# Optimization experiments

Measured on AMD Instinct MI355X. Metric: run time of the kernel, lower is better.

Reference implementation:

```python
import jax, jax.numpy as jnp
import numpy as np

N = 49104   # anchors (from hardcoded [2, 49104, 80] in source)
C = 80      # classes
K = 100     # max detections kept per class (fixed for jit-able output shapes)
SCORE_THRESH = 0.05
IOU_THRESH = 0.5


def setup_inputs() -> dict:
    key = jax.random.key(0)
    k1, k2 = jax.random.split(key)
    scores = jax.random.uniform(k1, (N, C), dtype=jnp.float32)
    # build valid xyxy boxes inside an ~800x800 image
    r = jax.random.uniform(k2, (N, 4), dtype=jnp.float32)
    x1 = r[:, 0] * 768.0
    y1 = r[:, 1] * 768.0
    w = r[:, 2] * 96.0 + 4.0
    h = r[:, 3] * 96.0 + 4.0
    boxes = jnp.stack([x1, y1, x1 + w, y1 + h], axis=1)
    return {"scores": scores, "boxes": boxes}


def _nms_all(scores, boxes):
    """Per-class greedy NMS, vectorized over classes via vmap.
    scores: [N, C], boxes: [N, 4] xyxy. Returns idxs/scs/valid each [C, K]."""
    areas = (boxes[:, 2] - boxes[:, 0]) * (boxes[:, 3] - boxes[:, 1])  # [N]

    def iou_vs_all(b, b_area):  # b: [4]
        ix1 = jnp.maximum(b[0], boxes[:, 0])
        iy1 = jnp.maximum(b[1], boxes[:, 1])
        ix2 = jnp.minimum(b[2], boxes[:, 2])
        iy2 = jnp.minimum(b[3], boxes[:, 3])
        inter = jnp.clip(ix2 - ix1, 0.0) * jnp.clip(iy2 - iy1, 0.0)
        return inter / (b_area + areas - inter + 1e-8)  # [N]

    def nms_one_class(s_c):  # s_c: [N]
        # score threshold (matches `scores > 0.05` masking in the torch loop)
        s0 = jnp.where(s_c > SCORE_THRESH, s_c, -jnp.inf)

        def step(s, _):
            idx = jnp.argmax(s)
            sc = s[idx]
            keep = jnp.isfinite(sc)  # anything left above threshold?
            ious = iou_vs_all(boxes[idx], areas[idx])
            suppress = (ious > IOU_THRESH) & keep
            s_next = jnp.where(suppress, -jnp.inf, s).at[idx].set(-jnp.inf)
            return s_next, (idx, sc, keep)

        _, (idxs, scs, keeps) = jax.lax.scan(step, s0, None, length=K)
        return idxs, scs, keeps  # each [K]

    return jax.vmap(nms_one_class)(scores.T)  # map over C classes


def reference(scores, boxes):
    idxs, scs, valids = _nms_all(scores, boxes)  # [C, K] each
    idxs = idxs.reshape(-1)                       # [C*K]
    valids = valids.reshape(-1)                   # [C*K] bool
    final_scores = jnp.where(valids, scs.reshape(-1), 0.0)        # [C*K]
    final_classes = jnp.repeat(jnp.arange(C, dtype=jnp.int32), K)  # [C*K]
    final_boxes = boxes[idxs] * valids[:, None].astype(boxes.dtype)  # [C*K, 4]
    return final_scores, final_classes, final_boxes, valids
```

## Files before the change

### kernel.cpp

```cpp
#include <hip/hip_runtime.h>
#include <math.h>
#include <stdint.h>

#define N_ANCH 49104
#define NCLS 80
#define KDET 100
#define CAP 256
#define TPB 256
#define NBINS 1024
#define NBLK 240
#define SUBCAP 32
#define THETA 0.996090f
#define QTOT (N_ANCH * NCLS / 4)
#define QPB (QTOT / NBLK)
#define JMAX 16

#define LIST_ELEMS ((size_t)NCLS * NBLK * SUBCAP)
#define SUBCNT_OFF (LIST_ELEMS * 8)
#define WS_NEED (SUBCNT_OFF + (size_t)NCLS * NBLK * 4)

__global__ __launch_bounds__(TPB) void collect_kernel(const float* __restrict__ scores,
                                                      uint64_t* __restrict__ list,
                                                      int* __restrict__ subcnt) {
    const int blk = blockIdx.x, tid = threadIdx.x;
    __shared__ int lcnt[NCLS];
    for (int c = tid; c < NCLS; c += TPB) lcnt[c] = 0;
    __syncthreads();
    const float4* sc4 = (const float4*)scores;
    const int q0 = blk * QPB;
    for (int q = q0 + tid; q < q0 + QPB; q += TPB) {
        float4 v = sc4[q];
        int n = q / 20;
        int c0 = 4 * (q % 20);
        float ss[4] = {v.x, v.y, v.z, v.w};
#pragma unroll
        for (int u = 0; u < 4; u++) {
            float s = ss[u];
            if (s > THETA) {
                int c = c0 + u;
                int p = atomicAdd(&lcnt[c], 1);
                if (p < SUBCAP) {
                    uint32_t bits = __float_as_uint(s);
                    list[((size_t)c * NBLK + blk) * SUBCAP + p] =
                        ((uint64_t)(~bits) << 16) | (uint64_t)n;
                }
            }
        }
    }
    __syncthreads();
    for (int c = tid; c < NCLS; c += TPB) subcnt[c * NBLK + blk] = lcnt[c];
}

struct ChunkShared {
    uint64_t keys[CAP];
    float4   rbox[CAP];
    float    ra[CAP], rs[CAP];
    uint64_t smat[CAP * (CAP / 64)];
    uint64_t lwbuf[CAP / 64];
    uint64_t s_kw[CAP / 64];
    int      s_cw[4];
    float4   kbox[KDET];
    float    kar[KDET], ksc[KDET];
};

__device__ __forceinline__ int process_chunk(ChunkShared& S, int tid, int M, int kc0,
                                             const float* __restrict__ boxes) {
    if (M <= 0) return kc0;
    const int lane = tid & 63, wid = tid >> 6;
    uint64_t key = (tid < M) ? S.keys[tid] : ~0ull;
    for (int k = 2; k <= CAP; k <<= 1) {
        for (int j = k >> 1; j > 0; j >>= 1) {
            uint64_t other;
            if (j >= 64) {
                __syncthreads();
                S.keys[tid] = key;
                __syncthreads();
                other = S.keys[tid ^ j];
            } else {
                other = (uint64_t)__shfl_xor((unsigned long long)key, j, 64);
            }
            const bool up = ((tid & k) == 0);
            const bool lower = ((tid & j) == 0);
            const uint64_t mn = key < other ? key : other;
            const uint64_t mx = key < other ? other : key;
            key = (lower == up) ? mn : mx;
        }
    }
    if (tid < M) {
        int n = (int)(key & 0xFFFFull);
        float4 bx = *(const float4*)(boxes + (size_t)n * 4);
        S.rbox[tid] = bx;
        S.ra[tid] = (bx.z - bx.x) * (bx.w - bx.y);
        S.rs[tid] = __uint_as_float(~((uint32_t)(key >> 16)));
    }
    __syncthreads();
    bool alive = (tid < M);
    if (alive && kc0 > 0) {
        float4 b = S.rbox[tid];
        float arb = S.ra[tid];
        for (int k2 = 0; k2 < kc0; k2++) {
            float4 kb = S.kbox[k2];
            float ix1 = fmaxf(kb.x, b.x), iy1 = fmaxf(kb.y, b.y);
            float ix2 = fminf(kb.z, b.z), iy2 = fminf(kb.w, b.w);
            float inter = fmaxf(ix2 - ix1, 0.0f) * fmaxf(iy2 - iy1, 0.0f);
            float iou = inter / (S.kar[k2] + arb - inter + 1e-8f);
            if (iou > 0.5f) { alive = false; break; }
        }
    }
    {
        uint64_t bal = __ballot(alive);
        if (lane == 0) S.lwbuf[wid] = bal;
    }
    __syncthreads();
    for (int p = wid; p < 10; p += 4) {
        const int vw = (int)((0x3333222110ull >> (4 * p)) & 0xF);
        const int ws = (int)((0x3210210100ull >> (4 * p)) & 0xF);
        const int i0 = vw << 6;
        if (i0 >= M) continue;
        const int i1 = min(M, i0 + 64);
        const int jj = (ws << 6) + lane;
        float4 bj = S.rbox[jj];
        float arj = S.ra[jj];
        for (int i = i0; i < i1; i++) {
            bool bit = false;
            if (jj < i) {
                float4 bi = S.rbox[i];
                float ari = S.ra[i];
                float ix1 = fmaxf(bj.x, bi.x), iy1 = fmaxf(bj.y, bi.y);
                float ix2 = fminf(bj.z, bi.z), iy2 = fminf(bj.w, bi.w);
                float inter = fmaxf(ix2 - ix1, 0.0f) * fmaxf(iy2 - iy1, 0.0f);
                float iou = inter / (arj + ari - inter + 1e-8f);
                bit = iou > 0.5f;
            }
            uint64_t bb = __ballot(bit);
            if (lane == 0) S.smat[((size_t)i << 2) + ws] = bb;
        }
    }
    __syncthreads();
    uint64_t st0 = 0, st1 = 0, st2 = 0, st3 = 0;
    if (tid < M) {
        st0 = S.smat[((size_t)tid << 2) + 0];
        if (wid >= 1) st1 = S.smat[((size_t)tid << 2) + 1];
        if (wid >= 2) st2 = S.smat[((size_t)tid << 2) + 2];
        if (wid >= 3) st3 = S.smat[((size_t)tid << 2) + 3];
    }
    bool kept = alive;
    bool converged = false;
    for (int it = 0; it < JMAX; it++) {
        uint64_t kb = __ballot(kept);
        if (lane == 0) S.s_kw[wid] = kb;
        __syncthreads();
        const uint64_t k0 = S.s_kw[0], k1 = S.s_kw[1], k2 = S.s_kw[2], k3 = S.s_kw[3];
        const bool sup = ((k0 & st0) | (k1 & st1) | (k2 & st2) | (k3 & st3)) != 0ull;
        const bool nk = alive && !sup;
        uint64_t cb = __ballot(nk != kept);
        if (lane == 0) S.s_cw[wid] = (cb != 0ull) ? 1 : 0;
        kept = nk;
        __syncthreads();
        if ((S.s_cw[0] | S.s_cw[1] | S.s_cw[2] | S.s_cw[3]) == 0) { converged = true; break; }
    }
    if (!converged) {
        if (tid == 0) {
            uint64_t lv[4] = {S.lwbuf[0], S.lwbuf[1], S.lwbuf[2], S.lwbuf[3]};
            uint64_t kw[4] = {0, 0, 0, 0};
            for (int i = 0; i < M; i++) {
                const int w = i >> 6, b = i & 63;
                if (!((lv[w] >> b) & 1ull)) continue;
                const uint64_t* row = &S.smat[(size_t)i << 2];
                uint64_t sup = kw[0] & row[0];
                if (w >= 1) sup |= kw[1] & row[1];
                if (w >= 2) sup |= kw[2] & row[2];
                if (w >= 3) sup |= kw[3] & row[3];
                if (!sup) kw[w] |= 1ull << b;
            }
            S.s_kw[0] = kw[0]; S.s_kw[1] = kw[1]; S.s_kw[2] = kw[2]; S.s_kw[3] = kw[3];
        }
        __syncthreads();
    }
    const uint64_t k0 = S.s_kw[0], k1 = S.s_kw[1], k2 = S.s_kw[2], k3 = S.s_kw[3];
    const int total = __popcll(k0) + __popcll(k1) + __popcll(k2) + __popcll(k3);
    const uint64_t mykw = (wid == 0) ? k0 : (wid == 1) ? k1 : (wid == 2) ? k2 : k3;
    if (tid < M && ((mykw >> lane) & 1ull)) {
        int rank = __popcll(mykw & ((1ull << lane) - 1ull));
        if (wid > 0) rank += __popcll(k0);
        if (wid > 1) rank += __popcll(k1);
        if (wid > 2) rank += __popcll(k2);
        const int r = kc0 + rank;
        if (r < KDET) { S.kbox[r] = S.rbox[tid]; S.kar[r] = S.ra[tid]; S.ksc[r] = S.rs[tid]; }
    }
    __syncthreads();
    return min(kc0 + total, KDET);
}

__global__ __launch_bounds__(TPB) void nms_final(const float* __restrict__ scores,
                                                 const float* __restrict__ boxes,
                                                 const uint64_t* __restrict__ list,
                                                 const int* __restrict__ subcnt,
                                                 int use_lists,
                                                 float* __restrict__ out) {
    const int c = blockIdx.x, tid = threadIdx.x;
    const int lane = tid & 63, wid = tid >> 6;
    __shared__ ChunkShared S;
    __shared__ int hist[NBINS];
    __shared__ int s_wtot[4];
    __shared__ int s_ov, s_cnt, s_lo;

    int kc = 0;
    bool fast = false;
    if (use_lists) {
        if (tid == 0) s_ov = 0;
        __syncthreads();
        int raw = (tid < NBLK) ? subcnt[c * NBLK + tid] : 0;
        if (raw > SUBCAP) atomicOr(&s_ov, 1);
        int v = min(raw, SUBCAP);
        int incl = v;
        for (int d = 1; d < 64; d <<= 1) {
            int o = __shfl_up(incl, d, 64);
            if (lane >= d) incl += o;
        }
        if (lane == 63) s_wtot[wid] = incl;
        __syncthreads();
        int woff = 0;
        for (int w = 0; w < wid; w++) woff += s_wtot[w];
        const int off = woff + incl - v;
        const int M0 = s_wtot[0] + s_wtot[1] + s_wtot[2] + s_wtot[3];
        fast = (s_ov == 0) && (M0 <= CAP);
        if (fast && tid < NBLK && v > 0) {
            const uint64_t* src = list + ((size_t)c * NBLK + tid) * SUBCAP;
            for (int k = 0; k < v; k++) S.keys[off + k] = src[k];
        }
        __syncthreads();
        if (fast) kc = process_chunk(S, tid, M0, 0, boxes);
    }
    if (kc < KDET) {
        const float hicut = fast ? THETA : 3.0e38f;
        if (!fast) kc = 0;
        for (int b = tid; b < NBINS; b += TPB) hist[b] = 0;
        __syncthreads();
        for (int n = tid; n < N_ANCH; n += TPB) {
            float s = scores[(size_t)n * NCLS + c];
            if (s > 0.05f && s <= hicut) {
                int b = (int)(s * 1024.0f);
                b = b < 0 ? 0 : (b > NBINS - 1 ? NBINS - 1 : b);
                atomicAdd(&hist[b], 1);
            }
        }
        __syncthreads();
        int hi = NBINS;
        while (hi > 0 && kc < KDET) {
            if (tid == 0) {
                int lo = hi, tot = 0;
                while (lo > 0 && tot + hist[lo - 1] <= CAP) { lo--; tot += hist[lo]; }
                if (lo == hi) lo = hi - 1;
                s_lo = lo; s_cnt = 0;
            }
            __syncthreads();
            const int lo = s_lo;
            for (int n = tid; n < N_ANCH; n += TPB) {
                float s = scores[(size_t)n * NCLS + c];
                if (s > 0.05f && s <= hicut) {
                    int b = (int)(s * 1024.0f);
                    b = b < 0 ? 0 : (b > NBINS - 1 ? NBINS - 1 : b);
                    if (b >= lo && b < hi) {
                        int p = atomicAdd(&s_cnt, 1);
                        if (p < CAP) {
                            uint32_t bits = __float_as_uint(s);
                            S.keys[p] = ((uint64_t)(~bits) << 16) | (uint64_t)n;
                        }
                    }
                }
            }
            __syncthreads();
            const int M2 = min(s_cnt, CAP);
            kc = process_chunk(S, tid, M2, kc, boxes);
            hi = lo;
        }
    }
    __syncthreads();

    float* o_sc = out;
    float* o_cl = out + NCLS * KDET;
    float* o_bx = out + 2 * NCLS * KDET;
    float* o_va = out + 6 * NCLS * KDET;
    for (int k = tid; k < KDET; k += TPB) {
        bool valid = k < kc;
        o_sc[c * KDET + k] = valid ? S.ksc[k] : 0.0f;
        o_cl[c * KDET + k] = (float)c;
        o_va[c * KDET + k] = valid ? 1.0f : 0.0f;
        float4 bo;
        if (valid) bo = S.kbox[k];
        else { bo.x = 0.0f; bo.y = 0.0f; bo.z = 0.0f; bo.w = 0.0f; }
        *(float4*)(o_bx + ((size_t)(c * KDET + k)) * 4) = bo;
    }
}

extern "C" void kernel_launch(void* const* d_in, const int* in_sizes, int n_in,
                              void* d_out, int out_size, void* d_ws, size_t ws_size,
                              hipStream_t stream) {
    const float* scores = (const float*)d_in[0];
    const float* boxes  = (const float*)d_in[1];
    float* out = (float*)d_out;

    uint64_t* list   = (uint64_t*)d_ws;
    int*      subcnt = (int*)((char*)d_ws + SUBCNT_OFF);
    const int use_lists = (ws_size >= WS_NEED) ? 1 : 0;

    if (use_lists) {
        collect_kernel<<<NBLK, TPB, 0, stream>>>(scores, list, subcnt);
    }
    nms_final<<<NCLS, TPB, 0, stream>>>(scores, boxes, list, subcnt, use_lists, out);
}
```

Baseline: 100.8 us.

## Prefetch boxes before sort and widen collect grid with unrolled loads

```diff
diff --git a/kernel.cpp b/kernel.cpp
--- a/kernel.cpp
+++ b/kernel.cpp
@@ -8,16 +8,35 @@
 #define CAP 256
 #define TPB 256
 #define NBINS 1024
-#define NBLK 240
-#define SUBCAP 32
+#define NBLK 512
+#define SUBCAP 16
 #define THETA 0.996090f
 #define QTOT (N_ANCH * NCLS / 4)
-#define QPB (QTOT / NBLK)
 #define JMAX 16
 
 #define LIST_ELEMS ((size_t)NCLS * NBLK * SUBCAP)
 #define SUBCNT_OFF (LIST_ELEMS * 8)
 #define WS_NEED (SUBCNT_OFF + (size_t)NCLS * NBLK * 4)
+
+__device__ __forceinline__ void collect_quad(int q, float4 v, int* lcnt,
+                                             uint64_t* __restrict__ list, int blk) {
+    const int n = q / 20;
+    const int c0 = 4 * (q % 20);
+    float ss[4] = {v.x, v.y, v.z, v.w};
+#pragma unroll
+    for (int u = 0; u < 4; u++) {
+        float s = ss[u];
+        if (s > THETA) {
+            int c = c0 + u;
+            int p = atomicAdd(&lcnt[c], 1);
+            if (p < SUBCAP) {
+                uint32_t bits = __float_as_uint(s);
+                list[((size_t)c * NBLK + blk) * SUBCAP + p] =
+                    ((uint64_t)(~bits) << 16) | (uint64_t)n;
+            }
+        }
+    }
+}
 
 __global__ __launch_bounds__(TPB) void collect_kernel(const float* __restrict__ scores,
                                                       uint64_t* __restrict__ list,
@@ -27,32 +46,23 @@
     for (int c = tid; c < NCLS; c += TPB) lcnt[c] = 0;
     __syncthreads();
     const float4* sc4 = (const float4*)scores;
-    const int q0 = blk * QPB;
-    for (int q = q0 + tid; q < q0 + QPB; q += TPB) {
-        float4 v = sc4[q];
-        int n = q / 20;
-        int c0 = 4 * (q % 20);
-        float ss[4] = {v.x, v.y, v.z, v.w};
-#pragma unroll
-        for (int u = 0; u < 4; u++) {
-            float s = ss[u];
-            if (s > THETA) {
-                int c = c0 + u;
-                int p = atomicAdd(&lcnt[c], 1);
-                if (p < SUBCAP) {
-                    uint32_t bits = __float_as_uint(s);
-                    list[((size_t)c * NBLK + blk) * SUBCAP + p] =
-                        ((uint64_t)(~bits) << 16) | (uint64_t)n;
-                }
-            }
-        }
-    }
+    const int stride = NBLK * TPB;
+    int q = blk * TPB + tid;
+    for (; q + 3 * stride < QTOT; q += 4 * stride) {
+        float4 v0 = sc4[q], v1 = sc4[q + stride], v2 = sc4[q + 2 * stride], v3 = sc4[q + 3 * stride];
+        collect_quad(q, v0, lcnt, list, blk);
+        collect_quad(q + stride, v1, lcnt, list, blk);
+        collect_quad(q + 2 * stride, v2, lcnt, list, blk);
+        collect_quad(q + 3 * stride, v3, lcnt, list, blk);
+    }
+    for (; q < QTOT; q += stride) collect_quad(q, sc4[q], lcnt, list, blk);
     __syncthreads();
     for (int c = tid; c < NCLS; c += TPB) subcnt[c * NBLK + blk] = lcnt[c];
 }
 
 struct ChunkShared {
     uint64_t keys[CAP];
+    float4   bxu[CAP];
     float4   rbox[CAP];
     float    ra[CAP], rs[CAP];
     uint64_t smat[CAP * (CAP / 64)];
@@ -68,6 +78,11 @@
     if (M <= 0) return kc0;
     const int lane = tid & 63, wid = tid >> 6;
     uint64_t key = (tid < M) ? S.keys[tid] : ~0ull;
+    float4 mybox;
+    if (tid < M) {
+        int n = (int)((key >> 8) & 0xFFFFull);
+        mybox = *(const float4*)(boxes + (size_t)n * 4);
+    }
     for (int k = 2; k <= CAP; k <<= 1) {
         for (int j = k >> 1; j > 0; j >>= 1) {
             uint64_t other;
@@ -86,12 +101,14 @@
             key = (lower == up) ? mn : mx;
         }
     }
+    if (tid < M) S.bxu[tid] = mybox;
+    __syncthreads();
     if (tid < M) {
-        int n = (int)(key & 0xFFFFull);
-        float4 bx = *(const float4*)(boxes + (size_t)n * 4);
+        int slot = (int)(key & 0xFFull);
+        float4 bx = S.bxu[slot];
         S.rbox[tid] = bx;
         S.ra[tid] = (bx.z - bx.x) * (bx.w - bx.y);
-        S.rs[tid] = __uint_as_float(~((uint32_t)(key >> 16)));
+        S.rs[tid] = __uint_as_float(~((uint32_t)(key >> 24)));
     }
     __syncthreads();
     bool alive = (tid < M);
@@ -210,9 +227,11 @@
     if (use_lists) {
         if (tid == 0) s_ov = 0;
         __syncthreads();
-        int raw = (tid < NBLK) ? subcnt[c * NBLK + tid] : 0;
-        if (raw > SUBCAP) atomicOr(&s_ov, 1);
-        int v = min(raw, SUBCAP);
+        const int raw0 = subcnt[c * NBLK + tid];
+        const int raw1 = subcnt[c * NBLK + TPB + tid];
+        if (raw0 > SUBCAP || raw1 > SUBCAP) atomicOr(&s_ov, 1);
+        const int v0 = min(raw0, SUBCAP), v1 = min(raw1, SUBCAP);
+        const int v = v0 + v1;
         int incl = v;
         for (int d = 1; d < 64; d <<= 1) {
             int o = __shfl_up(incl, d, 64);
@@ -225,9 +244,11 @@
         const int off = woff + incl - v;
         const int M0 = s_wtot[0] + s_wtot[1] + s_wtot[2] + s_wtot[3];
         fast = (s_ov == 0) && (M0 <= CAP);
-        if (fast && tid < NBLK && v > 0) {
-            const uint64_t* src = list + ((size_t)c * NBLK + tid) * SUBCAP;
-            for (int k = 0; k < v; k++) S.keys[off + k] = src[k];
+        if (fast) {
+            const uint64_t* src0 = list + ((size_t)c * NBLK + tid) * SUBCAP;
+            const uint64_t* src1 = list + ((size_t)c * NBLK + TPB + tid) * SUBCAP;
+            for (int k = 0; k < v0; k++) S.keys[off + k]      = (src0[k] << 8) | (uint64_t)(off + k);
+            for (int k = 0; k < v1; k++) S.keys[off + v0 + k] = (src1[k] << 8) | (uint64_t)(off + v0 + k);
         }
         __syncthreads();
         if (fast) kc = process_chunk(S, tid, M0, 0, boxes);
@@ -265,7 +286,7 @@
                         int p = atomicAdd(&s_cnt, 1);
                         if (p < CAP) {
                             uint32_t bits = __float_as_uint(s);
-                            S.keys[p] = ((uint64_t)(~bits) << 16) | (uint64_t)n;
+                            S.keys[p] = ((uint64_t)(~bits) << 24) | ((uint64_t)n << 8) | (uint64_t)p;
                         }
                     }
                 }
```

New measurement: 101.3 us. About the same (+0.5%).
